# Kernel optimization log

Hardware: AMD Instinct MI355X
Metric: run time of the kernel (lower is better)

The kernel has to match this reference:

```python
import jax, jax.numpy as jnp
import numpy as np

M0, M1 = 16, 16          # n_modes
C = 64                   # hidden_channels
B = 16                   # batch
H = W = 128              # spatial resolution
SCALE = C ** (-2)        # matches torch: scale * torch.rand(...)


def setup_inputs() -> dict:
    key = jax.random.key(0)
    kx, k0r, k0i, k1r, k1i = jax.random.split(key, 5)
    X = jax.random.normal(kx, (B, C, H, W), dtype=jnp.float32)
    wshape = (C, C, M0, M1)
    # torch.rand with cfloat draws U[0,1) for real and imag parts independently
    w0r = SCALE * jax.random.uniform(k0r, wshape, dtype=jnp.float32)
    w0i = SCALE * jax.random.uniform(k0i, wshape, dtype=jnp.float32)
    w1r = SCALE * jax.random.uniform(k1r, wshape, dtype=jnp.float32)
    w1i = SCALE * jax.random.uniform(k1i, wshape, dtype=jnp.float32)
    return {"X": X, "w0r": w0r, "w0i": w0i, "w1r": w1r, "w1i": w1i}


def reference(X, w0r, w0i, w1r, w1i):
    w0 = w0r + 1j * w0i                       # linear0: (C, C, M0, M1) complex
    w1 = w1r + 1j * w1i                       # linear1
    Xf = jnp.fft.rfftn(X, axes=(-2, -1), norm="forward")   # (B, C, H, W//2+1) complex
    # out[b,c] = sum_t weight[c,t] * Xf[b,t] on the two kept-mode corners
    top = jnp.einsum("ctxy,btxy->bcxy", w0, Xf[:, :, :M0, :M1])
    bot = jnp.einsum("ctxy,btxy->bcxy", w1, Xf[:, :, -M0:, :M1])
    Y = jnp.zeros_like(Xf)
    Y = Y.at[:, :, :M0, :M1].set(top)
    Y = Y.at[:, :, -M0:, :M1].set(bot)
    out = jnp.fft.irfftn(Y, axes=(-2, -1), s=(H, W), norm="forward")
    return out.astype(jnp.float32)
```

## Files before the change

kernel.cpp:

```cpp
#include <hip/hip_runtime.h>

#define PI2 6.28318530717958647692f

__global__ __launch_bounds__(256, 4) void k_fwd(const float* __restrict__ X,
                                                float* __restrict__ Xf) {
  __shared__ __attribute__((aligned(16))) float A2t[128 * 18 * 2];
  __shared__ __attribute__((aligned(16))) float Tt[64 * 16 * 2];
  const int plane = blockIdx.x;
  const int tid = threadIdx.x;
  const float* Xp = X + (size_t)plane * (128 * 128);

  #pragma unroll
  for (int k = 0; k < 4; ++k) {
    int idx = tid + k * 256;
    int h = idx >> 4, slot = idx & 15;
    int kx = slot ? slot : 16;
    float ang = -PI2 * (float)((kx * h) & 127) / 128.f;
    float s_, c_;
    __sincosf(ang, &s_, &c_);
    Tt[idx * 2] = c_; Tt[idx * 2 + 1] = s_;
  }
  __syncthreads();

  {
    const int w2 = tid & 63;
    const int kxq = tid >> 6;
    float ar[4][2], ai[4][2];
    #pragma unroll
    for (int j = 0; j < 4; ++j) {
      ar[j][0] = 0.f; ar[j][1] = 0.f; ai[j][0] = 0.f; ai[j][1] = 0.f;
    }
    float dc0 = 0.f, dc1 = 0.f;
    const float* colp = Xp + 2 * w2;

#define ROWSTEP(HH, TT_, BB_) do {                                           \
    float uex_ = (TT_).x + (BB_).x, uox_ = (TT_).x - (BB_).x;                \
    float uey_ = (TT_).y + (BB_).y, uoy_ = (TT_).y - (BB_).y;                \
    const float4* Trow_ = (const float4*)&Tt[(HH) * 32];                     \
    float4 e01_ = Trow_[kxq * 2];        \
    float4 e23_ = Trow_[kxq * 2 + 1];     \
    ar[0][0] = fmaf(uex_, e01_.x, ar[0][0]); ai[0][0] = fmaf(uex_, e01_.y, ai[0][0]); \
    ar[0][1] = fmaf(uey_, e01_.x, ar[0][1]); ai[0][1] = fmaf(uey_, e01_.y, ai[0][1]); \
    ar[1][0] = fmaf(uox_, e01_.z, ar[1][0]); ai[1][0] = fmaf(uox_, e01_.w, ai[1][0]); \
    ar[1][1] = fmaf(uoy_, e01_.z, ar[1][1]); ai[1][1] = fmaf(uoy_, e01_.w, ai[1][1]); \
    ar[2][0] = fmaf(uex_, e23_.x, ar[2][0]); ai[2][0] = fmaf(uex_, e23_.y, ai[2][0]); \
    ar[2][1] = fmaf(uey_, e23_.x, ar[2][1]); ai[2][1] = fmaf(uey_, e23_.y, ai[2][1]); \
    ar[3][0] = fmaf(uox_, e23_.z, ar[3][0]); ai[3][0] = fmaf(uox_, e23_.w, ai[3][0]); \
    ar[3][1] = fmaf(uoy_, e23_.z, ar[3][1]); ai[3][1] = fmaf(uoy_, e23_.w, ai[3][1]); \
    if (kxq == 0) { dc0 += uex_; dc1 += uey_; }            \
  } while (0)

    float2 p0t = *(const float2*)&colp[0 * 128];
    float2 p0b = *(const float2*)&colp[64 * 128];
    float2 p1t = *(const float2*)&colp[1 * 128];
    float2 p1b = *(const float2*)&colp[65 * 128];
    float2 p2t = *(const float2*)&colp[2 * 128];
    float2 p2b = *(const float2*)&colp[66 * 128];
    float2 p3t = *(const float2*)&colp[3 * 128];
    float2 p3b = *(const float2*)&colp[67 * 128];

    for (int h = 0; h < 64; h += 4) {
      float2 n0t, n0b, n1t, n1b, n2t, n2b, n3t, n3b;
      if (h < 60) {
        n0t = *(const float2*)&colp[(h + 4) * 128];
        n0b = *(const float2*)&colp[(h + 68) * 128];
        n1t = *(const float2*)&colp[(h + 5) * 128];
        n1b = *(const float2*)&colp[(h + 69) * 128];
        n2t = *(const float2*)&colp[(h + 6) * 128];
        n2b = *(const float2*)&colp[(h + 70) * 128];
        n3t = *(const float2*)&colp[(h + 7) * 128];
        n3b = *(const float2*)&colp[(h + 71) * 128];
      } else {
        n0t = make_float2(0.f, 0.f); n0b = n0t; n1t = n0t; n1b = n0t;
        n2t = n0t; n2b = n0t; n3t = n0t; n3b = n0t;
      }
      ROWSTEP(h, p0t, p0b);
      ROWSTEP(h + 1, p1t, p1b);
      ROWSTEP(h + 2, p2t, p2b);
      ROWSTEP(h + 3, p3t, p3b);
      p0t = n0t; p0b = n0b; p1t = n1t; p1b = n1b;
      p2t = n2t; p2b = n2b; p3t = n3t; p3b = n3b;
    }
#undef ROWSTEP

    #pragma unroll
    for (int j = 0; j < 4; ++j) {
      int s = kxq * 4 + j;
      int row = (s == 0) ? 16 : s;
      *(float2*)&A2t[((2 * w2) * 18 + row) * 2]     = make_float2(ar[j][0], ai[j][0]);
      *(float2*)&A2t[((2 * w2 + 1) * 18 + row) * 2] = make_float2(ar[j][1], ai[j][1]);
    }
    if (kxq == 0) {
      *(float2*)&A2t[((2 * w2) * 18) * 2]     = make_float2(dc0, 0.f);
      *(float2*)&A2t[((2 * w2 + 1) * 18) * 2] = make_float2(dc1, 0.f);
    }
  }
  __syncthreads();

  {
    const int kxi = tid >> 3;
    const int t = tid & 7;
    const int row = (kxi < 16) ? kxi : (32 - kxi);
    const float csign = (kxi < 16) ? 1.f : -1.f;
    const float s = (t & 1) ? -1.f : 1.f;
    float s0r, s0i, s1r, s1i;
    __sincosf(-PI2 * (float)t / 128.f, &s0i, &s0r);
    __sincosf(-PI2 * (float)(t + 8) / 128.f, &s1i, &s1r);
    float r0 = 0.f, i0 = 0.f, r1 = 0.f, i1 = 0.f;
    float E0r = 1.f, E0i = 0.f, E1r = 1.f, E1i = 0.f;
    #pragma unroll
    for (int half = 0; half < 2; ++half) {
      if (half == 1) {
        float c_, s_;
        __sincosf(-1.57079632679489662f * (float)t, &s_, &c_);
        E0r = c_; E0i = s_; E1r = c_; E1i = s_;
      }
      for (int w = half * 32; w < half * 32 + 32; ++w) {
        float2 a = *(const float2*)&A2t[(w * 18 + row) * 2];
        float2 b = *(const float2*)&A2t[((w + 64) * 18 + row) * 2];
        float ur = fmaf(s, b.x, a.x);
        float ui = csign * fmaf(s, b.y, a.y);
        r0 = fmaf(ur, E0r, r0); r0 = fmaf(-ui, E0i, r0);
        i0 = fmaf(ur, E0i, i0); i0 = fmaf(ui, E0r, i0);
        r1 = fmaf(ur, E1r, r1); r1 = fmaf(-ui, E1i, r1);
        i1 = fmaf(ur, E1i, i1); i1 = fmaf(ui, E1r, i1);
        float u0 = E0r * s0r - E0i * s0i; E0i = E0r * s0i + E0i * s0r; E0r = u0;
        float u1 = E1r * s1r - E1i * s1i; E1i = E1r * s1i + E1i * s1r; E1r = u1;
      }
    }
    const float sc = 1.f / 16384.f;
    float* base = Xf + (size_t)plane * 1024 + kxi * 32;
    *(float2*)&base[t * 2]       = make_float2(r0 * sc, i0 * sc);
    *(float2*)&base[(t + 8) * 2] = make_float2(r1 * sc, i1 * sc);
  }
}

__global__ __launch_bounds__(256, 2) void k_mix(const float* __restrict__ Xf,
                                                const float* __restrict__ w0r,
                                                const float* __restrict__ w0i,
                                                const float* __restrict__ w1r,
                                                const float* __restrict__ w1i,
                                                float* __restrict__ Y) {
  __shared__ __attribute__((aligned(16))) float Wl[4 * 32 * 16 * 4];
  const int bid = blockIdx.x;
  const int c2 = bid >> 8;
  const int x  = (bid >> 4) & 15;
  const int cg = bid & 15;
  const int c0 = cg * 4;
  const int kxi = c2 * 16 + x;
  const float* Wr_g = c2 ? w1r : w0r;
  const float* Wi_g = c2 ? w1i : w0i;
  const int tid = threadIdx.x;
  const int b = tid >> 4;
  const int y = tid & 15;

  #pragma unroll
  for (int k = 0; k < 16; ++k) {
    int idx = tid + k * 256;
    int y_ = idx & 15, t_ = (idx >> 4) & 63, c_ = idx >> 10;
    size_t ga = (((size_t)(c0 + c_) * 64 + t_) * 16 + x) * 16 + y_;
    int f2i = ((c_ * 32 + (t_ >> 1)) * 16 + y_) * 2 + (t_ & 1);
    *(float2*)&Wl[f2i * 2] = make_float2(Wr_g[ga], Wi_g[ga]);
  }
  __syncthreads();

  float aR[4] = {}, aI[4] = {};
  const float* xbase = Xf + ((size_t)b * 64) * 1024 + kxi * 32 + y * 2;
  for (int t8 = 0; t8 < 64; t8 += 8) {
    float2 xv[8];
    #pragma unroll
    for (int q = 0; q < 8; ++q)
      xv[q] = *(const float2*)&xbase[(size_t)(t8 + q) * 1024];
    #pragma unroll
    for (int p = 0; p < 4; ++p) {
      int t2 = (t8 >> 1) + p;
      float2 xe = xv[2 * p], xo = xv[2 * p + 1];
      #pragma unroll
      for (int cj = 0; cj < 4; ++cj) {
        float4 wv = *(const float4*)&Wl[((cj * 32 + t2) * 16 + y) * 4];
        aR[cj] = fmaf(xe.x, wv.x, aR[cj]); aR[cj] = fmaf(-xe.y, wv.y, aR[cj]);
        aI[cj] = fmaf(xe.x, wv.y, aI[cj]); aI[cj] = fmaf(xe.y, wv.x, aI[cj]);
        aR[cj] = fmaf(xo.x, wv.z, aR[cj]); aR[cj] = fmaf(-xo.y, wv.w, aR[cj]);
        aI[cj] = fmaf(xo.x, wv.w, aI[cj]); aI[cj] = fmaf(xo.y, wv.z, aI[cj]);
      }
    }
  }
  #pragma unroll
  for (int cj = 0; cj < 4; ++cj) {
    size_t ya = ((size_t)(b * 64 + c0 + cj)) * 1024 + kxi * 32 + y * 2;
    *(float2*)&Y[ya] = make_float2(aR[cj], aI[cj]);
  }
}

__global__ __launch_bounds__(256, 4) void k_inv(const float* __restrict__ Y,
                                                float* __restrict__ out) {
  __shared__ __attribute__((aligned(16))) float Yl[1024];
  __shared__ __attribute__((aligned(16))) float Mt[128 * 16 * 2];
  const int plane = blockIdx.x;
  const int tid = threadIdx.x;
  *(float4*)&Yl[tid * 4] = *(const float4*)&Y[(size_t)plane * 1024 + tid * 4];
  __syncthreads();

  {
    const int g = tid >> 6;
    const int h2 = tid & 63;
    float zr[2][4] = {}, zi[2][4] = {};
    float uw, uwi;
    __sincosf(PI2 * (float)h2 / 128.f, &uwi, &uw);
    const float4* Yl4 = (const float4*)Yl;
    float Tr = 1.f, Ti = 0.f;
    #pragma unroll 2
    for (int kxi = 0; kxi < 16; ++kxi) {
      float sgn = (kxi & 1) ? -1.f : 1.f;
      #pragma unroll
      for (int q = 0; q < 2; ++q) {
        float4 p = Yl4[kxi * 8 + g * 2 + q];
        float cr0 = p.x * Tr - p.y * Ti, ci0 = p.x * Ti + p.y * Tr;
        float cr1 = p.z * Tr - p.w * Ti, ci1 = p.z * Ti + p.w * Tr;
        zr[0][2*q]   += cr0; zi[0][2*q]   += ci0;
        zr[0][2*q+1] += cr1; zi[0][2*q+1] += ci1;
        zr[1][2*q]   = fmaf(sgn, cr0, zr[1][2*q]);   zi[1][2*q]   = fmaf(sgn, ci0, zi[1][2*q]);
        zr[1][2*q+1] = fmaf(sgn, cr1, zr[1][2*q+1]); zi[1][2*q+1] = fmaf(sgn, ci1, zi[1][2*q+1]);
      }
      float nr = Tr * uw - Ti * uwi, ni = Tr * uwi + Ti * uw;
      Tr = nr; Ti = ni;
    }
    __sincosf(PI2 * (float)((112 * h2) & 127) / 128.f, &Ti, &Tr);
    #pragma unroll 2
    for (int kxi = 16; kxi < 32; ++kxi) {
      float sgn = (kxi & 1) ? -1.f : 1.f;
      #pragma unroll
      for (int q = 0; q < 2; ++q) {
        float4 p = Yl4[kxi * 8 + g * 2 + q];
        float cr0 = p.x * Tr - p.y * Ti, ci0 = p.x * Ti + p.y * Tr;
        float cr1 = p.z * Tr - p.w * Ti, ci1 = p.z * Ti + p.w * Tr;
        zr[0][2*q]   += cr0; zi[0][2*q]   += ci0;
        zr[0][2*q+1] += cr1; zi[0][2*q+1] += ci1;
        zr[1][2*q]   = fmaf(sgn, cr0, zr[1][2*q]);   zi[1][2*q]   = fmaf(sgn, ci0, zi[1][2*q]);
        zr[1][2*q+1] = fmaf(sgn, cr1, zr[1][2*q+1]); zi[1][2*q+1] = fmaf(sgn, ci1, zi[1][2*q+1]);
      }
      float nr = Tr * uw - Ti * uwi, ni = Tr * uwi + Ti * uw;
      Tr = nr; Ti = ni;
    }
    #pragma unroll
    for (int hs = 0; hs < 2; ++hs) {
      int h = h2 + hs * 64;
      #pragma unroll
      for (int q = 0; q < 2; ++q) {
        int ky0 = g * 4 + 2 * q;
        float f0 = (ky0 == 0) ? 1.f : 2.f;
        float4 v = make_float4(f0 * zr[hs][2*q],   -f0 * zi[hs][2*q],
                               2.f * zr[hs][2*q+1], -2.f * zi[hs][2*q+1]);
        int f4i = h * 8 + ((g * 2 + q) ^ (h & 7));
        *(float4*)&Mt[f4i * 4] = v;
      }
    }
  }
  __syncthreads();

  {
    const int hp = tid >> 5;
    const int w2 = tid & 31;
    float C[16], S[16];
    {
      float cw, sw;
      __sincosf(PI2 * (float)w2 / 128.f, &sw, &cw);
      C[0] = 1.f; S[0] = 0.f;
      #pragma unroll
      for (int k = 1; k < 16; ++k) {
        C[k] = C[k - 1] * cw - S[k - 1] * sw;
        S[k] = C[k - 1] * sw + S[k - 1] * cw;
      }
    }
    float* op = out + (size_t)plane * (128 * 128);
    const float4* Mt4 = (const float4*)Mt;
    #pragma unroll 2
    for (int hj = 0; hj < 16; ++hj) {
      int h = hp * 16 + hj;
      float e = 0.f, o = 0.f, e2 = 0.f, o2 = 0.f;
      #pragma unroll
      for (int j = 0; j < 8; ++j) {
        float4 m = Mt4[h * 8 + (j ^ (h & 7))];
        int k0 = 2 * j, k1 = 2 * j + 1;
        e = fmaf(m.x, C[k0], e); e = fmaf(m.y, S[k0], e);
        o = fmaf(m.z, C[k1], o); o = fmaf(m.w, S[k1], o);
        if ((k0 & 2) == 0) { e2 = fmaf(m.x, C[k0], e2); e2 = fmaf(m.y, S[k0], e2); }
        else               { e2 = fmaf(-m.x, C[k0], e2); e2 = fmaf(-m.y, S[k0], e2); }
        if ((k1 & 2) == 0) { o2 = fmaf(m.w, C[k1], o2); o2 = fmaf(-m.z, S[k1], o2); }
        else               { o2 = fmaf(-m.w, C[k1], o2); o2 = fmaf(m.z, S[k1], o2); }
      }
      op[h * 128 + w2]      = e + o;
      op[h * 128 + w2 + 64] = e - o;
      op[h * 128 + w2 + 32] = e2 + o2;
      op[h * 128 + w2 + 96] = e2 - o2;
    }
  }
}

extern "C" void kernel_launch(void* const* d_in, const int* in_sizes, int n_in,
                              void* d_out, int out_size, void* d_ws, size_t ws_size,
                              hipStream_t stream) {
  const float* X   = (const float*)d_in[0];
  const float* w0r = (const float*)d_in[1];
  const float* w0i = (const float*)d_in[2];
  const float* w1r = (const float*)d_in[3];
  const float* w1i = (const float*)d_in[4];
  float* outp = (float*)d_out;
  float* Xf = (float*)d_ws;
  float* Yw = (float*)d_ws + (1u << 20);
  k_fwd<<<1024, 256, 0, stream>>>(X, Xf);
  k_mix<<<512, 256, 0, stream>>>(Xf, w0r, w0i, w1r, w1i, Yw);
  k_inv<<<1024, 256, 0, stream>>>(Yw, outp);
}
```

Measured before the change: 170.6 us.

## Stage input rows through double-buffered LDS with coalesced float4 loads; transpose A2t layout

The forward DFT stage now loads input rows cooperatively with 16-byte coalesced global loads into a double-buffered shared-memory tile, instead of each thread reading strided float2 columns straight from global memory. The intermediate A2t buffer is transposed to row-major by frequency with a padded stride, so results are stored as float4 and the second stage reads consecutive addresses. This aims to improve global-load efficiency and LDS bank behaviour. In exchange it adds a __syncthreads per 4-row chunk and extra shared memory, which may reduce occupancy.

```diff
diff --git a/kernel.cpp b/kernel.cpp
--- a/kernel.cpp
+++ b/kernel.cpp
@@ -4,8 +4,9 @@
 
 __global__ __launch_bounds__(256, 4) void k_fwd(const float* __restrict__ X,
                                                 float* __restrict__ Xf) {
-  __shared__ __attribute__((aligned(16))) float A2t[128 * 18 * 2];
+  __shared__ __attribute__((aligned(16))) float A2t[17 * 134 * 2];
   __shared__ __attribute__((aligned(16))) float Tt[64 * 16 * 2];
+  __shared__ __attribute__((aligned(16))) float Xc[2][8 * 128];
   const int plane = blockIdx.x;
   const int tid = threadIdx.x;
   const float* Xp = X + (size_t)plane * (128 * 128);
@@ -20,22 +21,31 @@
     __sincosf(ang, &s_, &c_);
     Tt[idx * 2] = c_; Tt[idx * 2 + 1] = s_;
   }
-  __syncthreads();
 
   {
     const int w2 = tid & 63;
     const int kxq = tid >> 6;
+    const int lrow = tid >> 5;
+    const int lcol = (tid & 31) * 4;
     float ar[4][2], ai[4][2];
     #pragma unroll
     for (int j = 0; j < 4; ++j) {
       ar[j][0] = 0.f; ar[j][1] = 0.f; ai[j][0] = 0.f; ai[j][1] = 0.f;
     }
     float dc0 = 0.f, dc1 = 0.f;
-    const float* colp = Xp + 2 * w2;
-
-#define ROWSTEP(HH, TT_, BB_) do {                                           \
-    float uex_ = (TT_).x + (BB_).x, uox_ = (TT_).x - (BB_).x;                \
-    float uey_ = (TT_).y + (BB_).y, uoy_ = (TT_).y - (BB_).y;                \
+
+    {
+      int rg = (lrow < 4) ? lrow : (60 + lrow);
+      float4 v = *(const float4*)&Xp[rg * 128 + lcol];
+      *(float4*)&Xc[0][lrow * 128 + lcol] = v;
+    }
+    __syncthreads();
+
+#define ROWSTEP(HH, JJ, XB) do {                                             \
+    float2 tt_ = *(const float2*)&(XB)[(JJ) * 128 + 2 * w2];                 \
+    float2 bb_ = *(const float2*)&(XB)[((JJ) + 4) * 128 + 2 * w2];           \
+    float uex_ = tt_.x + bb_.x, uox_ = tt_.x - bb_.x;                        \
+    float uey_ = tt_.y + bb_.y, uoy_ = tt_.y - bb_.y;                        \
     const float4* Trow_ = (const float4*)&Tt[(HH) * 32];                     \
     float4 e01_ = Trow_[kxq * 2];        \
     float4 e23_ = Trow_[kxq * 2 + 1];     \
@@ -50,36 +60,20 @@
     if (kxq == 0) { dc0 += uex_; dc1 += uey_; }            \
   } while (0)
 
-    float2 p0t = *(const float2*)&colp[0 * 128];
-    float2 p0b = *(const float2*)&colp[64 * 128];
-    float2 p1t = *(const float2*)&colp[1 * 128];
-    float2 p1b = *(const float2*)&colp[65 * 128];
-    float2 p2t = *(const float2*)&colp[2 * 128];
-    float2 p2b = *(const float2*)&colp[66 * 128];
-    float2 p3t = *(const float2*)&colp[3 * 128];
-    float2 p3b = *(const float2*)&colp[67 * 128];
-
-    for (int h = 0; h < 64; h += 4) {
-      float2 n0t, n0b, n1t, n1b, n2t, n2b, n3t, n3b;
-      if (h < 60) {
-        n0t = *(const float2*)&colp[(h + 4) * 128];
-        n0b = *(const float2*)&colp[(h + 68) * 128];
-        n1t = *(const float2*)&colp[(h + 5) * 128];
-        n1b = *(const float2*)&colp[(h + 69) * 128];
-        n2t = *(const float2*)&colp[(h + 6) * 128];
-        n2b = *(const float2*)&colp[(h + 70) * 128];
-        n3t = *(const float2*)&colp[(h + 7) * 128];
-        n3b = *(const float2*)&colp[(h + 71) * 128];
-      } else {
-        n0t = make_float2(0.f, 0.f); n0b = n0t; n1t = n0t; n1b = n0t;
-        n2t = n0t; n2b = n0t; n3t = n0t; n3b = n0t;
-      }
-      ROWSTEP(h, p0t, p0b);
-      ROWSTEP(h + 1, p1t, p1b);
-      ROWSTEP(h + 2, p2t, p2b);
-      ROWSTEP(h + 3, p3t, p3b);
-      p0t = n0t; p0b = n0b; p1t = n1t; p1b = n1b;
-      p2t = n2t; p2b = n2b; p3t = n3t; p3b = n3b;
+    for (int c = 0; c < 16; ++c) {
+      float4 nv;
+      if (c < 15) {
+        int rg = (lrow < 4) ? (4 * (c + 1) + lrow) : (60 + 4 * (c + 1) + lrow);
+        nv = *(const float4*)&Xp[rg * 128 + lcol];
+      }
+      const float* Xb = &Xc[c & 1][0];
+      ROWSTEP(4 * c,     0, Xb);
+      ROWSTEP(4 * c + 1, 1, Xb);
+      ROWSTEP(4 * c + 2, 2, Xb);
+      ROWSTEP(4 * c + 3, 3, Xb);
+      if (c < 15)
+        *(float4*)&Xc[(c + 1) & 1][lrow * 128 + lcol] = nv;
+      __syncthreads();
     }
 #undef ROWSTEP
 
@@ -87,12 +81,11 @@
     for (int j = 0; j < 4; ++j) {
       int s = kxq * 4 + j;
       int row = (s == 0) ? 16 : s;
-      *(float2*)&A2t[((2 * w2) * 18 + row) * 2]     = make_float2(ar[j][0], ai[j][0]);
-      *(float2*)&A2t[((2 * w2 + 1) * 18 + row) * 2] = make_float2(ar[j][1], ai[j][1]);
+      *(float4*)&A2t[(row * 134 + 2 * w2) * 2] =
+          make_float4(ar[j][0], ai[j][0], ar[j][1], ai[j][1]);
     }
     if (kxq == 0) {
-      *(float2*)&A2t[((2 * w2) * 18) * 2]     = make_float2(dc0, 0.f);
-      *(float2*)&A2t[((2 * w2 + 1) * 18) * 2] = make_float2(dc1, 0.f);
+      *(float4*)&A2t[(2 * w2) * 2] = make_float4(dc0, 0.f, dc1, 0.f);
     }
   }
   __syncthreads();
@@ -116,8 +109,8 @@
         E0r = c_; E0i = s_; E1r = c_; E1i = s_;
       }
       for (int w = half * 32; w < half * 32 + 32; ++w) {
-        float2 a = *(const float2*)&A2t[(w * 18 + row) * 2];
-        float2 b = *(const float2*)&A2t[((w + 64) * 18 + row) * 2];
+        float2 a = *(const float2*)&A2t[(row * 134 + w) * 2];
+        float2 b = *(const float2*)&A2t[(row * 134 + w + 64) * 2];
         float ur = fmaf(s, b.x, a.x);
         float ui = csign * fmaf(s, b.y, a.y);
         r0 = fmaf(ur, E0r, r0); r0 = fmaf(-ui, E0i, r0);
```

Result: faster. 161.7 us, median of 2 (-5.2%).
